# Kernel tuning notes

Measured on AMD Instinct MI355X. Metric: run time of the kernel, lower is better.

The kernel has to match this reference:

```python
import jax, jax.numpy as jnp
import numpy as np
import math

B, N, F_IN, F_OUT = 16, 2048, 256, 64


def setup_inputs() -> dict:
    key = jax.random.key(0)
    k1, k2, k3, k4 = jax.random.split(key, 4)
    x = jax.random.normal(k1, (B, N, F_IN), dtype=jnp.float32)
    adj = jax.random.randint(k2, (B, N, N), 0, 2, dtype=jnp.int32)
    stdv = 1.0 / math.sqrt(F_OUT)
    weight = jax.random.uniform(k3, (F_IN, F_OUT), dtype=jnp.float32, minval=-stdv, maxval=stdv)
    # weight2 stdv = 1/sqrt(1) = 1.0
    weight2 = jax.random.uniform(k4, (2 * F_OUT, 1), dtype=jnp.float32, minval=-1.0, maxval=1.0)
    return {"x": x, "adj": adj, "weight": weight, "weight2": weight2}


def reference(x, adj, weight, weight2):
    # h[b,n,o] = (x @ weight)  -- shared linear projection
    h = jnp.einsum("bni,io->bno", x, weight)
    Fo = weight.shape[1]
    # Split additive-attention vector: e_ij = relu(h_i . a_src + h_j . a_dst)
    # Mathematically identical to cat([h_i, h_j]) @ weight2 of the original.
    a_src = weight2[:Fo, 0]
    a_dst = weight2[Fo:, 0]
    s_src = jnp.einsum("bno,o->bn", h, a_src)  # [B, N]
    s_dst = jnp.einsum("bno,o->bn", h, a_dst)  # [B, N]
    e = jax.nn.relu(s_src[:, :, None] + s_dst[:, None, :])  # [B, N, N]
    NEG = jnp.float32(-9e15)
    scores = jnp.where(adj > 0, e, NEG)
    attention = jax.nn.softmax(scores, axis=2)  # softmax over neighbors j
    # dropout = 0.0 / eval mode -> identity
    out = jnp.einsum("bij,bjo->bio", attention, h)  # [B, N, F_OUT]
    return out
```

## Files before the change

### kernel.cpp

```cpp
#include <hip/hip_runtime.h>
#include <hip/hip_bf16.h>

#define BB 16
#define NN 2048
#define FIN 256
#define FO 64
#define CH 512

typedef __bf16 bf16x8 __attribute__((ext_vector_type(8)));
typedef __bf16 bf16x4 __attribute__((ext_vector_type(4)));
typedef float  f32x4  __attribute__((ext_vector_type(4)));
typedef int    i32x4  __attribute__((ext_vector_type(4)));

__global__ void k0_prep(const float* __restrict__ weight, const float* __restrict__ w2,
                        __bf16* __restrict__ Wt, float* __restrict__ vsrc,
                        float* __restrict__ vdst) {
    int t = threadIdx.x;
    for (int idx = t; idx < FIN * FO; idx += 256) {
        int k = idx >> 6, o = idx & 63;
        Wt[o * FIN + k] = (__bf16)weight[idx];
    }
    float a = 0.f, d = 0.f;
    for (int o = 0; o < FO; ++o) {
        float wv = weight[t * FO + o];
        a += wv * w2[o];
        d += wv * w2[FO + o];
    }
    vsrc[t] = a;
    vdst[t] = d;
}

__global__ __launch_bounds__(256) void k1_gemm(
    const float* __restrict__ x, const __bf16* __restrict__ Wt,
    const float* __restrict__ vsrc, const float* __restrict__ vdst,
    __bf16* __restrict__ hT, float* __restrict__ s_src, float* __restrict__ s_dst) {
    int lane = threadIdx.x & 63, w = threadIdx.x >> 6;
    int quad = lane >> 4, m = lane & 15;
    int Rbase = blockIdx.x * 64 + w * 16;
    int R = Rbase + m;
    const float* xr = x + (long)R * FIN;

    f32x4 acc[4] = {};
    float ps = 0.f, pd = 0.f;

#pragma unroll
    for (int k0 = 0; k0 < FIN; k0 += 32) {
        int kb = k0 + quad * 8;
        float4 x0 = *(const float4*)(xr + kb);
        float4 x1 = *(const float4*)(xr + kb + 4);
        float4 u0 = *(const float4*)(vsrc + kb);
        float4 u1 = *(const float4*)(vsrc + kb + 4);
        float4 t0 = *(const float4*)(vdst + kb);
        float4 t1 = *(const float4*)(vdst + kb + 4);
        ps += x0.x * u0.x + x0.y * u0.y + x0.z * u0.z + x0.w * u0.w +
              x1.x * u1.x + x1.y * u1.y + x1.z * u1.z + x1.w * u1.w;
        pd += x0.x * t0.x + x0.y * t0.y + x0.z * t0.z + x0.w * t0.w +
              x1.x * t1.x + x1.y * t1.y + x1.z * t1.z + x1.w * t1.w;
        bf16x8 bf = {(__bf16)x0.x, (__bf16)x0.y, (__bf16)x0.z, (__bf16)x0.w,
                     (__bf16)x1.x, (__bf16)x1.y, (__bf16)x1.z, (__bf16)x1.w};
#pragma unroll
        for (int ot = 0; ot < 4; ++ot) {
            bf16x8 af = *(const bf16x8*)(Wt + (ot * 16 + m) * FIN + kb);
            acc[ot] = __builtin_amdgcn_mfma_f32_16x16x32_bf16(af, bf, acc[ot], 0, 0, 0);
        }
    }
    ps += __shfl_xor(ps, 16);
    ps += __shfl_xor(ps, 32);
    pd += __shfl_xor(pd, 16);
    pd += __shfl_xor(pd, 32);
    if (quad == 0) {
        s_src[R] = ps;
        s_dst[R] = pd;
    }
    int b = R >> 11;
    int nb = Rbase & (NN - 1);
#pragma unroll
    for (int ot = 0; ot < 4; ++ot) {
#pragma unroll
        for (int r = 0; r < 4; ++r) {
            int o = ot * 16 + quad * 4 + r;
            hT[((long)b * FO + o) * NN + nb + m] = (__bf16)acc[ot][r];
        }
    }
}

__global__ __launch_bounds__(256) void k2_attn(
    const int* __restrict__ adj, const float* __restrict__ s_src,
    const float* __restrict__ s_dst, const __bf16* __restrict__ hT,
    float* __restrict__ out) {
    __shared__ __bf16 pbuf[4][16 * CH];
    int b = blockIdx.x >> 5;
    int i0 = (blockIdx.x & 31) << 6;
    int lane = threadIdx.x & 63, w = threadIdx.x >> 6;
    int quad = lane >> 4, m = lane & 15;
    int rowbase = i0 + w * 16;

    const float* sd = s_dst + b * NN;
    float mx = -3.0e38f;
    for (int j = lane; j < NN; j += 64) mx = fmaxf(mx, sd[j]);
#pragma unroll
    for (int off = 32; off >= 1; off >>= 1) mx = fmaxf(mx, __shfl_xor(mx, off));

    const float* ssp = s_src + b * NN + rowbase;
    const int* adjb = adj + ((long)b * NN + rowbase) * NN;
    const __bf16* hTb = hT + (long)b * FO * NN;
    __bf16* pb = pbuf[w];

    f32x4 acc[4] = {};
    float lp = 0.f;

    for (int jc = 0; jc < NN; jc += CH) {
        float4 sv0 = *(const float4*)(sd + jc + 4 * lane);
        float4 sv1 = *(const float4*)(sd + jc + 256 + 4 * lane);
#pragma unroll
        for (int r = 0; r < 16; ++r) {
            float sr = ssp[r];
            float M = fmaxf(sr + mx, 0.f);
            const int* ap = adjb + (long)r * NN + jc;
            i32x4 a0 = __builtin_nontemporal_load((const i32x4*)ap + lane);
            i32x4 a1 = __builtin_nontemporal_load((const i32x4*)(ap + 256) + lane);
            float p0 = (a0.x > 0) ? __expf(fmaxf(sr + sv0.x, 0.f) - M) : 0.f;
            float p1 = (a0.y > 0) ? __expf(fmaxf(sr + sv0.y, 0.f) - M) : 0.f;
            float p2 = (a0.z > 0) ? __expf(fmaxf(sr + sv0.z, 0.f) - M) : 0.f;
            float p3 = (a0.w > 0) ? __expf(fmaxf(sr + sv0.w, 0.f) - M) : 0.f;
            float p4 = (a1.x > 0) ? __expf(fmaxf(sr + sv1.x, 0.f) - M) : 0.f;
            float p5 = (a1.y > 0) ? __expf(fmaxf(sr + sv1.y, 0.f) - M) : 0.f;
            float p6 = (a1.z > 0) ? __expf(fmaxf(sr + sv1.z, 0.f) - M) : 0.f;
            float p7 = (a1.w > 0) ? __expf(fmaxf(sr + sv1.w, 0.f) - M) : 0.f;
            bf16x4 k0v = {(__bf16)p0, (__bf16)p1, (__bf16)p2, (__bf16)p3};
            bf16x4 k1v = {(__bf16)p4, (__bf16)p5, (__bf16)p6, (__bf16)p7};
            int g0 = lane >> 3, u = (lane & 7) * 4;
            *(bf16x4*)(pb + g0 * 512 + r * 32 + u) = k0v;
            *(bf16x4*)(pb + (8 + g0) * 512 + r * 32 + u) = k1v;
        }
#pragma unroll
        for (int ks = 0; ks < CH / 32; ++ks) {
            bf16x8 af = *(const bf16x8*)(pb + (ks * 16 + m) * 32 + quad * 8);
#pragma unroll
            for (int e = 0; e < 8; ++e) lp += (float)af[e];
            const __bf16* hb = hTb + jc + ks * 32 + quad * 8;
#pragma unroll
            for (int ot = 0; ot < 4; ++ot) {
                bf16x8 bf = *(const bf16x8*)(hb + (ot * 16 + m) * NN);
                acc[ot] = __builtin_amdgcn_mfma_f32_16x16x32_bf16(af, bf, acc[ot], 0, 0, 0);
            }
        }
    }

    lp += __shfl_xor(lp, 16);
    lp += __shfl_xor(lp, 32);

    float* outp = out + ((long)b * NN + rowbase) * FO;
#pragma unroll
    for (int r = 0; r < 4; ++r) {
        int orow = quad * 4 + r;
        float lr = __shfl(lp, orow);
        float inv = 1.0f / lr;
#pragma unroll
        for (int ot = 0; ot < 4; ++ot) {
            outp[(long)orow * FO + ot * 16 + m] = acc[ot][r] * inv;
        }
    }
}

extern "C" void kernel_launch(void* const* d_in, const int* in_sizes, int n_in,
                              void* d_out, int out_size, void* d_ws, size_t ws_size,
                              hipStream_t stream) {
    const float* x      = (const float*)d_in[0];
    const int*   adj    = (const int*)d_in[1];
    const float* weight = (const float*)d_in[2];
    const float* w2     = (const float*)d_in[3];
    float* out = (float*)d_out;

    char* ws = (char*)d_ws;
    __bf16* hT   = (__bf16*)ws;
    float* s_src = (float*)(ws + 4194304);
    float* s_dst = (float*)(ws + 4194304 + 131072);
    float* vsrc  = (float*)(ws + 4194304 + 262144);
    float* vdst  = (float*)(ws + 4194304 + 262144 + 1024);
    __bf16* Wt   = (__bf16*)(ws + 4194304 + 262144 + 2048);

    k0_prep<<<1, 256, 0, stream>>>(weight, w2, Wt, vsrc, vdst);
    k1_gemm<<<512, 256, 0, stream>>>(x, Wt, vsrc, vdst, hT, s_src, s_dst);
    k2_attn<<<512, 256, 0, stream>>>(adj, s_src, s_dst, hT, out);
}
```

Baseline: 478.4 us.

## Fuse weight prep into GEMM, use MFMA for row sums, shrink attention chunk

The single-block prep kernel is removed. Each GEMM block now transposes the weight into padded LDS and computes the folded attention vectors itself, which drops one launch and the serial single-block prologue. In the attention kernel the softmax denominator is computed with an MFMA against a ones vector instead of per-lane scalar adds plus shuffles. The column chunk is halved to 256, so there are more chunk iterations, each issuing fewer loads. The cost is redundant per-block weight preparation and an extra MFMA per k-step.

```diff
diff --git a/kernel.cpp b/kernel.cpp
--- a/kernel.cpp
+++ b/kernel.cpp
@@ -5,35 +5,41 @@
 #define NN 2048
 #define FIN 256
 #define FO 64
-#define CH 512
+#define PADW 264
+#define CH 256
 
 typedef __bf16 bf16x8 __attribute__((ext_vector_type(8)));
 typedef __bf16 bf16x4 __attribute__((ext_vector_type(4)));
 typedef float  f32x4  __attribute__((ext_vector_type(4)));
 typedef int    i32x4  __attribute__((ext_vector_type(4)));
 
-__global__ void k0_prep(const float* __restrict__ weight, const float* __restrict__ w2,
-                        __bf16* __restrict__ Wt, float* __restrict__ vsrc,
-                        float* __restrict__ vdst) {
+__global__ __launch_bounds__(256) void k1_gemm(
+    const float* __restrict__ x, const float* __restrict__ weight,
+    const float* __restrict__ w2,
+    __bf16* __restrict__ hT, float* __restrict__ s_src, float* __restrict__ s_dst) {
+    __shared__ __bf16 WtL[FO * PADW];
+    __shared__ float vsL[FIN], vdL[FIN];
     int t = threadIdx.x;
-    for (int idx = t; idx < FIN * FO; idx += 256) {
-        int k = idx >> 6, o = idx & 63;
-        Wt[o * FIN + k] = (__bf16)weight[idx];
+    {
+        const float4* wr = (const float4*)(weight + t * FO);
+        float a = 0.f, d = 0.f;
+#pragma unroll
+        for (int c = 0; c < 16; ++c) {
+            float4 v = wr[c];
+            int o = c * 4;
+            WtL[(o + 0) * PADW + t] = (__bf16)v.x;
+            WtL[(o + 1) * PADW + t] = (__bf16)v.y;
+            WtL[(o + 2) * PADW + t] = (__bf16)v.z;
+            WtL[(o + 3) * PADW + t] = (__bf16)v.w;
+            a += v.x * w2[o] + v.y * w2[o + 1] + v.z * w2[o + 2] + v.w * w2[o + 3];
+            d += v.x * w2[FO + o] + v.y * w2[FO + o + 1] +
+                 v.z * w2[FO + o + 2] + v.w * w2[FO + o + 3];
+        }
+        vsL[t] = a;
+        vdL[t] = d;
     }
-    float a = 0.f, d = 0.f;
-    for (int o = 0; o < FO; ++o) {
-        float wv = weight[t * FO + o];
-        a += wv * w2[o];
-        d += wv * w2[FO + o];
-    }
-    vsrc[t] = a;
-    vdst[t] = d;
-}
+    __syncthreads();
 
-__global__ __launch_bounds__(256) void k1_gemm(
-    const float* __restrict__ x, const __bf16* __restrict__ Wt,
-    const float* __restrict__ vsrc, const float* __restrict__ vdst,
-    __bf16* __restrict__ hT, float* __restrict__ s_src, float* __restrict__ s_dst) {
     int lane = threadIdx.x & 63, w = threadIdx.x >> 6;
     int quad = lane >> 4, m = lane & 15;
     int Rbase = blockIdx.x * 64 + w * 16;
@@ -48,10 +54,10 @@
         int kb = k0 + quad * 8;
         float4 x0 = *(const float4*)(xr + kb);
         float4 x1 = *(const float4*)(xr + kb + 4);
-        float4 u0 = *(const float4*)(vsrc + kb);
-        float4 u1 = *(const float4*)(vsrc + kb + 4);
-        float4 t0 = *(const float4*)(vdst + kb);
-        float4 t1 = *(const float4*)(vdst + kb + 4);
+        float4 u0 = *(const float4*)(vsL + kb);
+        float4 u1 = *(const float4*)(vsL + kb + 4);
+        float4 t0 = *(const float4*)(vdL + kb);
+        float4 t1 = *(const float4*)(vdL + kb + 4);
         ps += x0.x * u0.x + x0.y * u0.y + x0.z * u0.z + x0.w * u0.w +
               x1.x * u1.x + x1.y * u1.y + x1.z * u1.z + x1.w * u1.w;
         pd += x0.x * t0.x + x0.y * t0.y + x0.z * t0.z + x0.w * t0.w +
@@ -60,7 +66,7 @@
                      (__bf16)x1.x, (__bf16)x1.y, (__bf16)x1.z, (__bf16)x1.w};
 #pragma unroll
         for (int ot = 0; ot < 4; ++ot) {
-            bf16x8 af = *(const bf16x8*)(Wt + (ot * 16 + m) * FIN + kb);
+            bf16x8 af = *(const bf16x8*)(WtL + (ot * 16 + m) * PADW + kb);
             acc[ot] = __builtin_amdgcn_mfma_f32_16x16x32_bf16(af, bf, acc[ot], 0, 0, 0);
         }
     }
@@ -107,37 +113,30 @@
     __bf16* pb = pbuf[w];
 
     f32x4 acc[4] = {};
-    float lp = 0.f;
+    f32x4 accL = {};
+    const bf16x8 ones = {(__bf16)1.f, (__bf16)1.f, (__bf16)1.f, (__bf16)1.f,
+                         (__bf16)1.f, (__bf16)1.f, (__bf16)1.f, (__bf16)1.f};
+    int g0 = lane >> 3, u = (lane & 7) * 4;
 
     for (int jc = 0; jc < NN; jc += CH) {
-        float4 sv0 = *(const float4*)(sd + jc + 4 * lane);
-        float4 sv1 = *(const float4*)(sd + jc + 256 + 4 * lane);
+        float4 sv = *(const float4*)(sd + jc + 4 * lane);
 #pragma unroll
         for (int r = 0; r < 16; ++r) {
             float sr = ssp[r];
             float M = fmaxf(sr + mx, 0.f);
-            const int* ap = adjb + (long)r * NN + jc;
-            i32x4 a0 = __builtin_nontemporal_load((const i32x4*)ap + lane);
-            i32x4 a1 = __builtin_nontemporal_load((const i32x4*)(ap + 256) + lane);
-            float p0 = (a0.x > 0) ? __expf(fmaxf(sr + sv0.x, 0.f) - M) : 0.f;
-            float p1 = (a0.y > 0) ? __expf(fmaxf(sr + sv0.y, 0.f) - M) : 0.f;
-            float p2 = (a0.z > 0) ? __expf(fmaxf(sr + sv0.z, 0.f) - M) : 0.f;
-            float p3 = (a0.w > 0) ? __expf(fmaxf(sr + sv0.w, 0.f) - M) : 0.f;
-            float p4 = (a1.x > 0) ? __expf(fmaxf(sr + sv1.x, 0.f) - M) : 0.f;
-            float p5 = (a1.y > 0) ? __expf(fmaxf(sr + sv1.y, 0.f) - M) : 0.f;
-            float p6 = (a1.z > 0) ? __expf(fmaxf(sr + sv1.z, 0.f) - M) : 0.f;
-            float p7 = (a1.w > 0) ? __expf(fmaxf(sr + sv1.w, 0.f) - M) : 0.f;
-            bf16x4 k0v = {(__bf16)p0, (__bf16)p1, (__bf16)p2, (__bf16)p3};
-            bf16x4 k1v = {(__bf16)p4, (__bf16)p5, (__bf16)p6, (__bf16)p7};
-            int g0 = lane >> 3, u = (lane & 7) * 4;
-            *(bf16x4*)(pb + g0 * 512 + r * 32 + u) = k0v;
-            *(bf16x4*)(pb + (8 + g0) * 512 + r * 32 + u) = k1v;
+            i32x4 a0 = __builtin_nontemporal_load(
+                (const i32x4*)(adjb + (long)r * NN + jc) + lane);
+            float p0 = (a0.x > 0) ? __expf(fmaxf(sr + sv.x, 0.f) - M) : 0.f;
+            float p1 = (a0.y > 0) ? __expf(fmaxf(sr + sv.y, 0.f) - M) : 0.f;
+            float p2 = (a0.z > 0) ? __expf(fmaxf(sr + sv.z, 0.f) - M) : 0.f;
+            float p3 = (a0.w > 0) ? __expf(fmaxf(sr + sv.w, 0.f) - M) : 0.f;
+            bf16x4 kv = {(__bf16)p0, (__bf16)p1, (__bf16)p2, (__bf16)p3};
+            *(bf16x4*)(pb + g0 * 512 + r * 32 + u) = kv;
         }
 #pragma unroll
         for (int ks = 0; ks < CH / 32; ++ks) {
-            bf16x8 af = *(const bf16x8*)(pb + (ks * 16 + m) * 32 + quad * 8);
-#pragma unroll
-            for (int e = 0; e < 8; ++e) lp += (float)af[e];
+            bf16x8 af = *(const bf16x8*)(pb + ks * 512 + m * 32 + quad * 8);
+            accL = __builtin_amdgcn_mfma_f32_16x16x32_bf16(af, ones, accL, 0, 0, 0);
             const __bf16* hb = hTb + jc + ks * 32 + quad * 8;
 #pragma unroll
             for (int ot = 0; ot < 4; ++ot) {
@@ -147,15 +146,11 @@
         }
     }
 
-    lp += __shfl_xor(lp, 16);
-    lp += __shfl_xor(lp, 32);
-
     float* outp = out + ((long)b * NN + rowbase) * FO;
 #pragma unroll
     for (int r = 0; r < 4; ++r) {
         int orow = quad * 4 + r;
-        float lr = __shfl(lp, orow);
-        float inv = 1.0f / lr;
+        float inv = 1.0f / accL[r];
 #pragma unroll
         for (int ot = 0; ot < 4; ++ot) {
             outp[(long)orow * FO + ot * 16 + m] = acc[ot][r] * inv;
@@ -176,11 +171,7 @@
     __bf16* hT   = (__bf16*)ws;
     float* s_src = (float*)(ws + 4194304);
     float* s_dst = (float*)(ws + 4194304 + 131072);
-    float* vsrc  = (float*)(ws + 4194304 + 262144);
-    float* vdst  = (float*)(ws + 4194304 + 262144 + 1024);
-    __bf16* Wt   = (__bf16*)(ws + 4194304 + 262144 + 2048);
 
-    k0_prep<<<1, 256, 0, stream>>>(weight, w2, Wt, vsrc, vdst);
-    k1_gemm<<<512, 256, 0, stream>>>(x, Wt, vsrc, vdst, hT, s_src, s_dst);
+    k1_gemm<<<512, 256, 0, stream>>>(x, weight, w2, hT, s_src, s_dst);
     k2_attn<<<512, 256, 0, stream>>>(adj, s_src, s_dst, hT, out);
 }
```

Result: no change. 476.9 us (-0.3%).
